# Optimization experiments

Hardware: AMD Instinct MI355X
Metric: run time of the kernel (lower is better)

The kernel has to match this reference:

```python
import jax, jax.numpy as jnp
import numpy as np

D_IN = 1024
D_OUT = 1024
NUM_HEADS = 16
HEAD_DIM = D_OUT // NUM_HEADS


def setup_inputs() -> dict:
    key = jax.random.key(0)
    ks = jax.random.split(key, 6)
    B, S = 2, 2048
    x = jax.random.normal(ks[0], (B, S, D_IN), dtype=jnp.float32)
    # nn.Linear stores weight as [out, in]; y = x @ W.T
    scale_in = 1.0 / np.sqrt(D_IN)
    w_query = jax.random.uniform(ks[1], (D_OUT, D_IN), jnp.float32, -scale_in, scale_in)
    w_key = jax.random.uniform(ks[2], (D_OUT, D_IN), jnp.float32, -scale_in, scale_in)
    w_value = jax.random.uniform(ks[3], (D_OUT, D_IN), jnp.float32, -scale_in, scale_in)
    scale_out = 1.0 / np.sqrt(D_OUT)
    w_out = jax.random.uniform(ks[4], (D_OUT, D_OUT), jnp.float32, -scale_out, scale_out)
    b_out = jax.random.uniform(ks[5], (D_OUT,), jnp.float32, -scale_out, scale_out)
    return {"x": x, "w_query": w_query, "w_key": w_key, "w_value": w_value,
            "w_out": w_out, "b_out": b_out}


def reference(x, w_query, w_key, w_value, w_out, b_out):
    B, S, _ = x.shape
    H, Dh = NUM_HEADS, HEAD_DIM
    # projections (no qkv bias), split heads -> [B, H, S, Dh]
    q = (x @ w_query.T).reshape(B, S, H, Dh).transpose(0, 2, 1, 3)
    k = (x @ w_key.T).reshape(B, S, H, Dh).transpose(0, 2, 1, 3)
    v = (x @ w_value.T).reshape(B, S, H, Dh).transpose(0, 2, 1, 3)
    # explicit [B, H, S, S] scores with causal mask (matches masked_fill(triu,-inf))
    scores = jnp.einsum('bhqd,bhkd->bhqk', q, k)
    causal = jnp.tril(jnp.ones((S, S), dtype=bool))  # True = keep
    scores = jnp.where(causal, scores, -jnp.inf)
    attn = jax.nn.softmax(scores / np.sqrt(Dh).astype(np.float32), axis=-1)
    # dropout p=0.0 -> identity
    ctx = jnp.einsum('bhqk,bhkd->bhqd', attn, v)  # [B, H, S, Dh]
    ctx = ctx.transpose(0, 2, 1, 3).reshape(B, S, H * Dh)
    return ctx @ w_out.T + b_out
```

## Files before the change

kernel.cpp:

```cpp
#include <hip/hip_runtime.h>
#include <hip/hip_bf16.h>

typedef __attribute__((ext_vector_type(8))) short short8;
typedef __attribute__((ext_vector_type(4))) short short4_t;
typedef __attribute__((ext_vector_type(8))) float f32x8;
typedef __attribute__((ext_vector_type(4))) float f32x4;

#define MFMA16(a, b, c) __builtin_amdgcn_mfma_f32_16x16x32_bf16((a), (b), (c), 0, 0, 0)


static __device__ __forceinline__ short f2bf(float f) {
    __hip_bfloat16 h = __float2bfloat16(f);
    return *reinterpret_cast<short*>(&h);
}

static __device__ __forceinline__ void g2l16(const void* g, void* l) {
    __builtin_amdgcn_global_load_lds(
        (const __attribute__((address_space(1))) void*)g,
        (__attribute__((address_space(3))) void*)l,
        16, 0, 0);
}

__global__ __launch_bounds__(256) void cvt_kernel(
    const float* __restrict__ x,  const float* __restrict__ wq,
    const float* __restrict__ wk, const float* __restrict__ wv,
    const float* __restrict__ wo, __hip_bfloat16* __restrict__ ws)
{
    const size_t e = ((size_t)blockIdx.x * 256 + threadIdx.x) * 8;
    const float* src;
    __hip_bfloat16* dst;
    size_t off;
    if (e < 4194304)      { src = x;  dst = ws + 16777216; off = e; }
    else if (e < 5242880) { src = wq; dst = ws + 20971520; off = e - 4194304; }
    else if (e < 6291456) { src = wk; dst = ws + 20971520 + 1048576; off = e - 5242880; }
    else if (e < 7340032) { src = wv; dst = ws + 20971520 + 2097152; off = e - 6291456; }
    else                  { src = wo; dst = ws + 24117248; off = e - 7340032; }

    f32x8 v = *reinterpret_cast<const f32x8*>(src + off);
    short8 o;
#pragma unroll
    for (int j = 0; j < 8; ++j) o[j] = f2bf(v[j]);
    *reinterpret_cast<short8*>(reinterpret_cast<short*>(dst) + off) = o;
}

__global__ __launch_bounds__(256) void qkv_gemm_kernel(
    const __hip_bfloat16* __restrict__ xbf_,
    const __hip_bfloat16* __restrict__ wqkv_,
    __hip_bfloat16* __restrict__ qkv_out)
{
    const int bid = blockIdx.x;
    const int xcd = bid & 7, kb = bid >> 3;
    const int mBlk = xcd * 4 + (kb / 24);
    const int nBlk = kb % 24;

    const int tid  = threadIdx.x;
    const int lane = tid & 63;
    const int wid  = tid >> 6;
    const int l16  = lane & 15;
    const int lhi  = lane >> 4;
    const int wr = wid >> 1, wc = wid & 1;

    const short* A = reinterpret_cast<const short*>(xbf_);
    const short* Bm = reinterpret_cast<const short*>(wqkv_);
    const int r0A = mBlk * 128, r0B = nBlk * 128;

    __shared__ __align__(16) short sA[128 * 64];
    __shared__ __align__(16) short sB[128 * 64];

    f32x4 acc[4][4] = {};

    for (int kk = 0; kk < 1024; kk += 64) {
#pragma unroll
        for (int it = 0; it < 4; ++it) {
            const int G = it * 256 + tid;
            const int row = G >> 3, gs = G & 7;
            const int gl = gs ^ (row & 7);
            short* lp = sA + (size_t)(it * 256 + wid * 64) * 8;
            g2l16(A + (size_t)(r0A + row) * 1024 + kk + gl * 8, lp);
        }
#pragma unroll
        for (int it = 0; it < 4; ++it) {
            const int G = it * 256 + tid;
            const int row = G >> 3, gs = G & 7;
            const int gl = gs ^ (row & 7);
            short* lp = sB + (size_t)(it * 256 + wid * 64) * 8;
            g2l16(Bm + (size_t)(r0B + row) * 1024 + kk + gl * 8, lp);
        }
        __syncthreads();

#pragma unroll
        for (int ks = 0; ks < 2; ++ks) {
            short8 a[4], b[4];
#pragma unroll
            for (int i = 0; i < 4; ++i) {
                const int row = wr * 64 + i * 16 + l16;
                const int sg = (ks * 4 + lhi) ^ (row & 7);
                a[i] = *reinterpret_cast<const short8*>(&sA[row * 64 + sg * 8]);
            }
#pragma unroll
            for (int j = 0; j < 4; ++j) {
                const int row = wc * 64 + j * 16 + l16;
                const int sg = (ks * 4 + lhi) ^ (row & 7);
                b[j] = *reinterpret_cast<const short8*>(&sB[row * 64 + sg * 8]);
            }
#pragma unroll
            for (int i = 0; i < 4; ++i)
#pragma unroll
                for (int j = 0; j < 4; ++j)
                    acc[i][j] = MFMA16(a[i], b[j], acc[i][j]);
        }
        __syncthreads();
    }

    const int nTileBase = nBlk * 128 + wc * 64;
    const int mat = (nTileBase >> 10);
    __hip_bfloat16* dst = qkv_out + (size_t)mat * 4194304;
    const int mBase = r0A + wr * 64;

    if (mat < 2) {
#pragma unroll
        for (int i = 0; i < 4; ++i)
#pragma unroll
            for (int j = 0; j < 4; ++j)
#pragma unroll
                for (int r = 0; r < 4; ++r) {
                    const int mRow = mBase + i * 16 + lhi * 4 + r;
                    const int nCol = (nTileBase + j * 16 + l16) & 1023;
                    const int bb = mRow >> 11, s = mRow & 2047;
                    const int h = nCol >> 6, d = nCol & 63;
                    dst[(((size_t)(bb * 16 + h) * 2048 + s) << 6) + d] =
                        __float2bfloat16(acc[i][j][r]);
                }
    } else {
#pragma unroll
        for (int i = 0; i < 4; ++i) {
            const int mRow0 = mBase + i * 16 + lhi * 4;
            const int bb = mRow0 >> 11, s0 = mRow0 & 2047;
#pragma unroll
            for (int j = 0; j < 4; ++j) {
                const int nCol = (nTileBase + j * 16 + l16) & 1023;
                const int h = nCol >> 6, d = nCol & 63;
                short4_t v4;
#pragma unroll
                for (int r = 0; r < 4; ++r) v4[r] = f2bf(acc[i][j][r]);
                *reinterpret_cast<short4_t*>(
                    reinterpret_cast<short*>(dst) +
                    (((size_t)(bb * 16 + h) * 64 + d) << 11) + s0) = v4;
            }
        }
    }
}

__global__ __launch_bounds__(256) void attn_kernel(
    const __hip_bfloat16* __restrict__ qkv,
    __hip_bfloat16* __restrict__ ctx)
{
    const int tid  = threadIdx.x;
    const int lane = tid & 63;
    const int wid  = tid >> 6;
    const int l16 = lane & 15;
    const int lhi = lane >> 4;

    const int bid = blockIdx.x;
    const int xcd = bid & 7, idx = bid >> 3;
    const int h4 = idx & 3, tg = idx >> 2;
    const int bh = xcd * 4 + h4;
    const int qtBase = (31 - tg) * 4;
    const int qt = qtBase + wid;
    const int q0 = qt * 16;

    const short* Q  = reinterpret_cast<const short*>(qkv) + (size_t)bh * 131072;
    const short* K  = Q + 4194304;
    const short* Vt = Q + 8388608;

    __shared__ __align__(16) short sK[2][64 * 64];
    __shared__ __align__(16) short sV[2][64 * 64];
    __shared__ __align__(16) short p_lds_all[4][16 * 72];
    short* p_lds = p_lds_all[wid];

    const int bb = bh >> 4, h = bh & 15;
    const float SCL = 0.125f * 1.44269504f;

    short8 qf[2];
    qf[0] = *reinterpret_cast<const short8*>(Q + (size_t)(q0 + l16) * 64 + lhi * 8);
    qf[1] = *reinterpret_cast<const short8*>(Q + (size_t)(q0 + l16) * 64 + 32 + lhi * 8);

    f32x4 oacc[4] = {};
    float lsum[4] = {};

    const int ns_blk = ((qtBase + 3) * 16 + 16 + 63) >> 6;

    auto stage = [&](int buf, int kv0) {
#pragma unroll
        for (int it = 0; it < 2; ++it) {
            const int G = it * 256 + tid;
            const int row = G >> 3, gs = G & 7;
            const int gl = gs ^ (row & 7);
            g2l16(K + (size_t)(kv0 + row) * 64 + gl * 8, &sK[buf][(size_t)G * 8]);
            g2l16(Vt + (size_t)row * 2048 + kv0 + gl * 8, &sV[buf][(size_t)G * 8]);
        }
    };

    stage(0, 0);
    asm volatile("s_waitcnt vmcnt(0)" ::: "memory");
    __syncthreads();

    int cur = 0;
#pragma unroll 1
    for (int st = 0; st < ns_blk; ++st) {
        const int kv0 = st * 64;

        if (st + 1 < ns_blk) stage(cur ^ 1, kv0 + 64);

        f32x4 sc[4];
#pragma unroll
        for (int nt = 0; nt < 4; ++nt) {
            f32x4 s = {};
#pragma unroll
            for (int ks = 0; ks < 2; ++ks) {
                const int row = nt * 16 + l16;
                const int sg = (ks * 4 + lhi) ^ (row & 7);
                short8 kb = *reinterpret_cast<const short8*>(&sK[cur][row * 64 + sg * 8]);
                s = MFMA16(qf[ks], kb, s);
            }
            sc[nt] = s;
        }

        const bool need_mask = (kv0 + 63) > q0;
#pragma unroll
        for (int r = 0; r < 4; ++r) {
            const int row = lhi * 4 + r;
            const int qrow = q0 + row;
#pragma unroll
            for (int nt = 0; nt < 4; ++nt) {
                float sv = sc[nt][r] * SCL;
                if (need_mask && (kv0 + nt * 16 + l16) > qrow) sv = -1.0e38f;
                const float p = exp2f(sv);
                lsum[r] += p;
                p_lds[row * 72 + nt * 16 + l16] = f2bf(p);
            }
        }
        asm volatile("s_waitcnt lgkmcnt(0)" ::: "memory");

#pragma unroll
        for (int ks = 0; ks < 2; ++ks) {
            short8 pf = *reinterpret_cast<const short8*>(
                &p_lds[l16 * 72 + ks * 32 + lhi * 8]);
#pragma unroll
            for (int dt = 0; dt < 4; ++dt) {
                const int row = dt * 16 + l16;
                const int sg = (ks * 4 + lhi) ^ (row & 7);
                short8 vb = *reinterpret_cast<const short8*>(&sV[cur][row * 64 + sg * 8]);
                oacc[dt] = MFMA16(pf, vb, oacc[dt]);
            }
        }

        asm volatile("s_waitcnt vmcnt(0)" ::: "memory");
        __syncthreads();
        cur ^= 1;
    }

    float rinv[4];
#pragma unroll
    for (int r = 0; r < 4; ++r) {
        float rs = lsum[r];
        rs += __shfl_xor(rs, 1);
        rs += __shfl_xor(rs, 2);
        rs += __shfl_xor(rs, 4);
        rs += __shfl_xor(rs, 8);
        rinv[r] = 1.0f / rs;
    }
#pragma unroll
    for (int dt = 0; dt < 4; ++dt)
#pragma unroll
        for (int r = 0; r < 4; ++r) {
            const int q = q0 + lhi * 4 + r;
            ctx[((size_t)bb * 2048 + q) * 1024 + h * 64 + dt * 16 + l16] =
                __float2bfloat16(oacc[dt][r] * rinv[r]);
        }
}

__global__ __launch_bounds__(256) void out_gemm_kernel(
    const __hip_bfloat16* __restrict__ ctx,
    const __hip_bfloat16* __restrict__ wobf,
    const float* __restrict__ bo,
    float* __restrict__ out)
{
    const int bid = blockIdx.x;
    const int xcd = bid & 7, kb = bid >> 3;
    const int mBlk = xcd * 4 + (kb >> 3);
    const int nBlk = kb & 7;

    const int tid  = threadIdx.x;
    const int lane = tid & 63;
    const int wid  = tid >> 6;
    const int l16  = lane & 15;
    const int lhi  = lane >> 4;
    const int wr = wid >> 1, wc = wid & 1;

    const short* A = reinterpret_cast<const short*>(ctx);
    const short* Bm = reinterpret_cast<const short*>(wobf);
    const int r0A = mBlk * 128, r0B = nBlk * 128;

    __shared__ __align__(16) short sA[128 * 64];
    __shared__ __align__(16) short sB[128 * 64];

    f32x4 acc[4][4] = {};

    for (int kk = 0; kk < 1024; kk += 64) {
#pragma unroll
        for (int it = 0; it < 4; ++it) {
            const int G = it * 256 + tid;
            const int row = G >> 3, gs = G & 7;
            const int gl = gs ^ (row & 7);
            short* lp = sA + (size_t)(it * 256 + wid * 64) * 8;
            g2l16(A + (size_t)(r0A + row) * 1024 + kk + gl * 8, lp);
        }
#pragma unroll
        for (int it = 0; it < 4; ++it) {
            const int G = it * 256 + tid;
            const int row = G >> 3, gs = G & 7;
            const int gl = gs ^ (row & 7);
            short* lp = sB + (size_t)(it * 256 + wid * 64) * 8;
            g2l16(Bm + (size_t)(r0B + row) * 1024 + kk + gl * 8, lp);
        }
        __syncthreads();

#pragma unroll
        for (int ks = 0; ks < 2; ++ks) {
            short8 a[4], b[4];
#pragma unroll
            for (int i = 0; i < 4; ++i) {
                const int row = wr * 64 + i * 16 + l16;
                const int sg = (ks * 4 + lhi) ^ (row & 7);
                a[i] = *reinterpret_cast<const short8*>(&sA[row * 64 + sg * 8]);
            }
#pragma unroll
            for (int j = 0; j < 4; ++j) {
                const int row = wc * 64 + j * 16 + l16;
                const int sg = (ks * 4 + lhi) ^ (row & 7);
                b[j] = *reinterpret_cast<const short8*>(&sB[row * 64 + sg * 8]);
            }
#pragma unroll
            for (int i = 0; i < 4; ++i)
#pragma unroll
                for (int j = 0; j < 4; ++j)
                    acc[i][j] = MFMA16(a[i], b[j], acc[i][j]);
        }
        __syncthreads();
    }

    const int mBase = r0A + wr * 64;
    const int nBase = r0B + wc * 64;
#pragma unroll
    for (int i = 0; i < 4; ++i)
#pragma unroll
        for (int j = 0; j < 4; ++j)
#pragma unroll
            for (int r = 0; r < 4; ++r) {
                const int mRow = mBase + i * 16 + lhi * 4 + r;
                const int nCol = nBase + j * 16 + l16;
                out[(size_t)mRow * 1024 + nCol] = acc[i][j][r] + bo[nCol];
            }
}

extern "C" void kernel_launch(void* const* d_in, const int* in_sizes, int n_in,
                              void* d_out, int out_size, void* d_ws, size_t ws_size,
                              hipStream_t stream) {
    const float* x  = (const float*)d_in[0];
    const float* wq = (const float*)d_in[1];
    const float* wk = (const float*)d_in[2];
    const float* wv = (const float*)d_in[3];
    const float* wo = (const float*)d_in[4];
    const float* bo = (const float*)d_in[5];

    __hip_bfloat16* ws = (__hip_bfloat16*)d_ws;
    __hip_bfloat16* ctx  = ws + 12582912;
    __hip_bfloat16* xbf  = ws + 16777216;
    __hip_bfloat16* wqkv = ws + 20971520;
    __hip_bfloat16* wobf = ws + 24117248;
    float* out = (float*)d_out;

    cvt_kernel<<<4096, 256, 0, stream>>>(x, wq, wk, wv, wo, ws);
    qkv_gemm_kernel<<<768, 256, 0, stream>>>(xbf, wqkv, ws);
    attn_kernel<<<1024, 256, 0, stream>>>(ws, ctx);
    out_gemm_kernel<<<256, 256, 0, stream>>>(ctx, wobf, bo, out);
}
```

Baseline: 121.9 us.

## Fold softmax scale into Q projection and widen attention blocks to eight waves

The softmax scale (including log2e) is folded into the Q projection epilogue, which removes the per-score multiply in attention. The attention kernel now runs 512-thread blocks of eight waves over 128 query rows, so each staged K/V tile serves twice as many queries. Waves skip KV tiles that lie entirely above their causal diagonal and mask only on the diagonal tile. QK^T is computed transposed so the P writes become packed 8-byte stores and the row-sum reduction needs fewer shuffles. The costs are more waves contending at each barrier and load imbalance inside a block, because its waves have different causal lengths.

Result: no change. 119.7 us (-1.8%).

```diff
diff --git a/kernel.cpp b/kernel.cpp
--- a/kernel.cpp
+++ b/kernel.cpp
@@ -12,6 +12,10 @@
 static __device__ __forceinline__ short f2bf(float f) {
     __hip_bfloat16 h = __float2bfloat16(f);
     return *reinterpret_cast<short*>(&h);
+}
+
+static __device__ __forceinline__ unsigned pack2bf(float lo, float hi) {
+    return ((unsigned)f2bf(lo) & 0xffffu) | ((unsigned)f2bf(hi) << 16);
 }
 
 static __device__ __forceinline__ void g2l16(const void* g, void* l) {
@@ -118,6 +122,7 @@
     const int mBase = r0A + wr * 64;
 
     if (mat < 2) {
+        const float qscl = (mat == 0) ? 0.18033688f : 1.0f;
 #pragma unroll
         for (int i = 0; i < 4; ++i)
 #pragma unroll
@@ -129,7 +134,7 @@
                     const int bb = mRow >> 11, s = mRow & 2047;
                     const int h = nCol >> 6, d = nCol & 63;
                     dst[(((size_t)(bb * 16 + h) * 2048 + s) << 6) + d] =
-                        __float2bfloat16(acc[i][j][r]);
+                        __float2bfloat16(acc[i][j][r] * qscl);
                 }
     } else {
 #pragma unroll
@@ -151,7 +156,7 @@
     }
 }
 
-__global__ __launch_bounds__(256) void attn_kernel(
+__global__ __launch_bounds__(512, 4) void attn_kernel(
     const __hip_bfloat16* __restrict__ qkv,
     __hip_bfloat16* __restrict__ ctx)
 {
@@ -165,9 +170,11 @@
     const int xcd = bid & 7, idx = bid >> 3;
     const int h4 = idx & 3, tg = idx >> 2;
     const int bh = xcd * 4 + h4;
-    const int qtBase = (31 - tg) * 4;
-    const int qt = qtBase + wid;
+    const int g  = 15 - tg;
+    const int qt = g * 8 + wid;
     const int q0 = qt * 16;
+    const int sd = q0 >> 6;
+    const int ns_blk = 2 * g + 2;
 
     const short* Q  = reinterpret_cast<const short*>(qkv) + (size_t)bh * 131072;
     const short* K  = Q + 4194304;
@@ -175,83 +182,86 @@
 
     __shared__ __align__(16) short sK[2][64 * 64];
     __shared__ __align__(16) short sV[2][64 * 64];
-    __shared__ __align__(16) short p_lds_all[4][16 * 72];
+    __shared__ __align__(16) short p_lds_all[8][16 * 72];
     short* p_lds = p_lds_all[wid];
 
     const int bb = bh >> 4, h = bh & 15;
-    const float SCL = 0.125f * 1.44269504f;
 
     short8 qf[2];
     qf[0] = *reinterpret_cast<const short8*>(Q + (size_t)(q0 + l16) * 64 + lhi * 8);
     qf[1] = *reinterpret_cast<const short8*>(Q + (size_t)(q0 + l16) * 64 + 32 + lhi * 8);
 
     f32x4 oacc[4] = {};
-    float lsum[4] = {};
-
-    const int ns_blk = ((qtBase + 3) * 16 + 16 + 63) >> 6;
-
+    float lsum = 0.0f;
+
+    const int srow = tid >> 3, sgs = tid & 7;
+    const int sgl = sgs ^ (srow & 7);
     auto stage = [&](int buf, int kv0) {
-#pragma unroll
-        for (int it = 0; it < 2; ++it) {
-            const int G = it * 256 + tid;
-            const int row = G >> 3, gs = G & 7;
-            const int gl = gs ^ (row & 7);
-            g2l16(K + (size_t)(kv0 + row) * 64 + gl * 8, &sK[buf][(size_t)G * 8]);
-            g2l16(Vt + (size_t)row * 2048 + kv0 + gl * 8, &sV[buf][(size_t)G * 8]);
-        }
+        g2l16(K + (size_t)(kv0 + srow) * 64 + sgl * 8, &sK[buf][(size_t)tid * 8]);
+        g2l16(Vt + (size_t)srow * 2048 + kv0 + sgl * 8, &sV[buf][(size_t)tid * 8]);
     };
 
     stage(0, 0);
     asm volatile("s_waitcnt vmcnt(0)" ::: "memory");
     __syncthreads();
 
+    const int r7 = l16 & 7;
     int cur = 0;
 #pragma unroll 1
     for (int st = 0; st < ns_blk; ++st) {
         const int kv0 = st * 64;
-
         if (st + 1 < ns_blk) stage(cur ^ 1, kv0 + 64);
 
-        f32x4 sc[4];
-#pragma unroll
-        for (int nt = 0; nt < 4; ++nt) {
-            f32x4 s = {};
+        if (st <= sd) {
+            f32x4 sc[4];
+#pragma unroll
+            for (int nt = 0; nt < 4; ++nt) {
+                f32x4 s = {};
+#pragma unroll
+                for (int ks = 0; ks < 2; ++ks) {
+                    const int sg = (ks * 4 + lhi) ^ r7;
+                    short8 kb = *reinterpret_cast<const short8*>(
+                        &sK[cur][(nt * 16 + l16) * 64 + sg * 8]);
+                    s = MFMA16(kb, qf[ks], s);
+                }
+                sc[nt] = s;
+            }
+
+            if (st == sd) {
+#pragma unroll
+                for (int nt = 0; nt < 4; ++nt) {
+                    const int kvb = kv0 + nt * 16 + lhi * 4;
+                    const int qrow = q0 + l16;
+#pragma unroll
+                    for (int r = 0; r < 4; ++r)
+                        if (kvb + r > qrow) sc[nt][r] = -1.0e38f;
+                }
+            }
+#pragma unroll
+            for (int nt = 0; nt < 4; ++nt) {
+                const float p0 = exp2f(sc[nt][0]);
+                const float p1 = exp2f(sc[nt][1]);
+                const float p2 = exp2f(sc[nt][2]);
+                const float p3 = exp2f(sc[nt][3]);
+                lsum += (p0 + p1) + (p2 + p3);
+                uint2 w;
+                w.x = pack2bf(p0, p1);
+                w.y = pack2bf(p2, p3);
+                *reinterpret_cast<uint2*>(&p_lds[l16 * 72 + nt * 16 + lhi * 4]) = w;
+            }
+            asm volatile("s_waitcnt lgkmcnt(0)" ::: "memory");
+
 #pragma unroll
             for (int ks = 0; ks < 2; ++ks) {
-                const int row = nt * 16 + l16;
-                const int sg = (ks * 4 + lhi) ^ (row & 7);
-                short8 kb = *reinterpret_cast<const short8*>(&sK[cur][row * 64 + sg * 8]);
-                s = MFMA16(qf[ks], kb, s);
-            }
-            sc[nt] = s;
-        }
-
-        const bool need_mask = (kv0 + 63) > q0;
-#pragma unroll
-        for (int r = 0; r < 4; ++r) {
-            const int row = lhi * 4 + r;
-            const int qrow = q0 + row;
-#pragma unroll
-            for (int nt = 0; nt < 4; ++nt) {
-                float sv = sc[nt][r] * SCL;
-                if (need_mask && (kv0 + nt * 16 + l16) > qrow) sv = -1.0e38f;
-                const float p = exp2f(sv);
-                lsum[r] += p;
-                p_lds[row * 72 + nt * 16 + l16] = f2bf(p);
-            }
-        }
-        asm volatile("s_waitcnt lgkmcnt(0)" ::: "memory");
-
-#pragma unroll
-        for (int ks = 0; ks < 2; ++ks) {
-            short8 pf = *reinterpret_cast<const short8*>(
-                &p_lds[l16 * 72 + ks * 32 + lhi * 8]);
-#pragma unroll
-            for (int dt = 0; dt < 4; ++dt) {
-                const int row = dt * 16 + l16;
-                const int sg = (ks * 4 + lhi) ^ (row & 7);
-                short8 vb = *reinterpret_cast<const short8*>(&sV[cur][row * 64 + sg * 8]);
-                oacc[dt] = MFMA16(pf, vb, oacc[dt]);
+                short8 pf = *reinterpret_cast<const short8*>(
+                    &p_lds[l16 * 72 + ks * 32 + lhi * 8]);
+#pragma unroll
+                for (int dt = 0; dt < 4; ++dt) {
+                    const int sg = (ks * 4 + lhi) ^ r7;
+                    short8 vb = *reinterpret_cast<const short8*>(
+                        &sV[cur][(dt * 16 + l16) * 64 + sg * 8]);
+                    oacc[dt] = MFMA16(pf, vb, oacc[dt]);
+                }
             }
         }
 
@@ -260,16 +270,14 @@
         cur ^= 1;
     }
 
+    float rs = lsum;
+    rs += __shfl_xor(rs, 16);
+    rs += __shfl_xor(rs, 32);
+    const float rinvq = 1.0f / rs;
     float rinv[4];
 #pragma unroll
-    for (int r = 0; r < 4; ++r) {
-        float rs = lsum[r];
-        rs += __shfl_xor(rs, 1);
-        rs += __shfl_xor(rs, 2);
-        rs += __shfl_xor(rs, 4);
-        rs += __shfl_xor(rs, 8);
-        rinv[r] = 1.0f / rs;
-    }
+    for (int r = 0; r < 4; ++r) rinv[r] = __shfl(rinvq, lhi * 4 + r);
+
 #pragma unroll
     for (int dt = 0; dt < 4; ++dt)
 #pragma unroll
@@ -383,6 +391,6 @@
 
     cvt_kernel<<<4096, 256, 0, stream>>>(x, wq, wk, wv, wo, ws);
     qkv_gemm_kernel<<<768, 256, 0, stream>>>(xbf, wqkv, ws);
-    attn_kernel<<<1024, 256, 0, stream>>>(ws, ctx);
+    attn_kernel<<<512, 512, 0, stream>>>(ws, ctx);
     out_gemm_kernel<<<256, 256, 0, stream>>>(ctx, wobf, bo, out);
 }
```
